# Kernel tuning notes

Hardware: AMD Instinct MI355X
Metric: run time of the kernel (lower is better)

Reference implementation:

```python
import jax, jax.numpy as jnp
import numpy as np

ROPE_BASE = 1000000.0
EPS = 1e-6
N_HEADS = 8


def apply_rope(x, base=ROPE_BASE):
    # x: [b, s, h, d]
    b, s, h, d = x.shape
    half = d // 2
    theta = 1.0 / base ** (2 * jnp.arange(half) / d)          # [half]
    angles = jnp.arange(s)[:, None] * theta[None, :]          # [s, half]
    cos = jnp.cos(angles)[None, :, None, :]                   # [1, s, 1, half]
    sin = jnp.sin(angles)[None, :, None, :]
    x1, x2 = jnp.split(x, 2, axis=-1)
    return jnp.concatenate([x1 * cos - x2 * sin, x1 * sin + x2 * cos], axis=-1)


def setup_inputs() -> dict:
    key = jax.random.key(0)
    ks = jax.random.split(key, 5)
    b, s, dim = 2, 4096, 512
    x = jax.random.normal(ks[0], (b, s, dim), dtype=jnp.float32)
    scale = jnp.ones((dim,), dtype=jnp.float32)
    init = 1.0 / np.sqrt(dim)
    Wq = jax.random.normal(ks[1], (dim, dim), dtype=jnp.float32) * init
    Wk = jax.random.normal(ks[2], (dim, dim), dtype=jnp.float32) * init
    Wv = jax.random.normal(ks[3], (dim, dim), dtype=jnp.float32) * init
    Wo = jax.random.normal(ks[4], (dim, dim), dtype=jnp.float32) * init
    return {"x": x, "scale": scale, "Wq": Wq, "Wk": Wk, "Wv": Wv, "Wo": Wo}


def reference(x, scale, Wq, Wk, Wv, Wo):
    b, s, dim = x.shape
    h = N_HEADS
    dh = dim // h
    # RMSNorm (use_fast_variance=False path)
    variance = jnp.mean(x ** 2, axis=-1, keepdims=True)
    x_norm = x / jnp.sqrt(variance + EPS) * scale
    # Projections (flax Linear: y = x @ kernel, kernel [in, out])
    q = (x_norm @ Wq).reshape(b, s, h, dh)
    k = (x_norm @ Wk).reshape(b, s, h, dh)
    v = (x_norm @ Wv).reshape(b, s, h, dh)
    q = apply_rope(q)
    k = apply_rope(k)
    scores = jnp.einsum('bthd,bshd->bhts', q, k) / jnp.sqrt(jnp.float32(dh))
    mask = jnp.triu(jnp.full((s, s), -jnp.inf, dtype=jnp.float32), k=1)
    scores = scores + mask[None, None, :, :]
    attn = jax.nn.softmax(scores, axis=-1)
    out = jnp.einsum('bhts,bshd->bthd', attn, v).reshape(b, s, dim)
    return out @ Wo
```

## Files before the change

### kernel.cpp

```cpp
#include <hip/hip_runtime.h>
#include <hip/hip_bf16.h>

typedef _Float16 f16;
typedef _Float16 f16x4 __attribute__((ext_vector_type(4)));
typedef _Float16 f16x8 __attribute__((ext_vector_type(8)));
typedef float f32x4 __attribute__((ext_vector_type(4)));

#define S_LEN 4096
#define DIM   512
#define NH    8
#define DH    64
#define BATCH 2
#define BHDIM (BATCH*NH)

#define QSCALE 0.18033688011112042f

__device__ __forceinline__ void gld16(const f16* g, f16* l) {
#if __has_builtin(__builtin_amdgcn_global_load_lds)
  __builtin_amdgcn_global_load_lds((const __attribute__((address_space(1))) void*)g,
                                   (__attribute__((address_space(3))) void*)l, 16, 0, 0);
#else
  *(f16x8*)l = *(const f16x8*)g;
#endif
}

__device__ __forceinline__ float fexp2(float x) {
#if __has_builtin(__builtin_amdgcn_exp2f)
  return __builtin_amdgcn_exp2f(x);
#else
  return exp2f(x);
#endif
}

__global__ __launch_bounds__(256) void rmsnorm_kernel(
    const float* __restrict__ x, const float* __restrict__ scale,
    f16* __restrict__ xn) {
  int row = blockIdx.x;
  int tid = threadIdx.x;
  const float* xr = x + (size_t)row * DIM;
  float2 v = *(const float2*)(xr + tid*2);
  float ss = v.x*v.x + v.y*v.y;
  #pragma unroll
  for (int off = 32; off > 0; off >>= 1) ss += __shfl_down(ss, off);
  __shared__ float red[4];
  if ((tid & 63) == 0) red[tid >> 6] = ss;
  __syncthreads();
  float tot = red[0] + red[1] + red[2] + red[3];
  float inv = rsqrtf(tot * (1.0f/DIM) + 1e-6f);
  float2 s = *(const float2*)(scale + tid*2);
  xn[(size_t)row*DIM + tid*2+0] = (f16)(v.x*inv*s.x);
  xn[(size_t)row*DIM + tid*2+1] = (f16)(v.y*inv*s.y);
}

__global__ void transpose_kernel(const float* __restrict__ Wq,
                                 const float* __restrict__ Wk,
                                 const float* __restrict__ Wv,
                                 const float* __restrict__ Wo,
                                 f16* __restrict__ wt_qkv, f16* __restrict__ wo_t) {
  __shared__ f16 tile[32][33];
  int mat = blockIdx.z;
  const float* src = (mat == 0) ? Wq : (mat == 1) ? Wk : (mat == 2) ? Wv : Wo;
  f16* dst = (mat < 3) ? (wt_qkv + (size_t)mat*DIM*DIM) : wo_t;
  int k0 = blockIdx.y * 32, n0 = blockIdx.x * 32;
  int tx = threadIdx.x, ty = threadIdx.y;
  #pragma unroll
  for (int i = 0; i < 32; i += 8)
    tile[ty+i][tx] = (f16)src[(size_t)(k0+ty+i)*DIM + n0+tx];
  __syncthreads();
  #pragma unroll
  for (int i = 0; i < 32; i += 8)
    dst[(size_t)(n0+ty+i)*DIM + k0+tx] = tile[tx][ty+i];
}

__global__ __launch_bounds__(256) void rope_table_kernel(float* __restrict__ ctab,
                                                         float* __restrict__ stab) {
  int idx = blockIdx.x*256 + threadIdx.x;
  int t = idx >> 5, d = idx & 31;
  float theta = exp2f(-(float)d * (19.931568569324174f / 32.0f));
  float sv, cv;
  sincosf((float)t * theta, &sv, &cv);
  ctab[idx] = cv; stab[idx] = sv;
}

__device__ __forceinline__ void gemm128_acc(
    const f16* __restrict__ A, const f16* __restrict__ Bt,
    int m0, int n0, f16* As, f16* Bs, f32x4 (&acc)[4][4]) {
  const int tid = threadIdx.x;
  const int wave = tid >> 6, lane = tid & 63;
  const int l16 = lane & 15, quad = lane >> 4;
  const int mrow = (wave & 1) * 64, ncol = (wave >> 1) * 64;
  const int srow = tid >> 3;
  const int gc = (tid & 7) ^ ((tid >> 3) & 7);

  for (int k0 = 0; k0 < DIM; k0 += 64) {
    if (k0) __syncthreads();
    #pragma unroll
    for (int i = 0; i < 4; i++) {
      gld16(A  + (size_t)(m0 + i*32 + srow)*DIM + k0 + gc*8, As + i*2048 + tid*8);
      gld16(Bt + (size_t)(n0 + i*32 + srow)*DIM + k0 + gc*8, Bs + i*2048 + tid*8);
    }
    __syncthreads();
    #pragma unroll
    for (int kc = 0; kc < 2; kc++) {
      f16x8 a[4], b[4];
      #pragma unroll
      for (int mt = 0; mt < 4; mt++) {
        int row = mrow + mt*16 + l16;
        a[mt] = *(const f16x8*)(As + row*64 + (((quad + 4*kc) ^ (l16 & 7)) * 8));
      }
      #pragma unroll
      for (int nt = 0; nt < 4; nt++) {
        int row = ncol + nt*16 + l16;
        b[nt] = *(const f16x8*)(Bs + row*64 + (((quad + 4*kc) ^ (l16 & 7)) * 8));
      }
      #pragma unroll
      for (int mt = 0; mt < 4; mt++)
        #pragma unroll
        for (int nt = 0; nt < 4; nt++)
          acc[mt][nt] = __builtin_amdgcn_mfma_f32_16x16x32_f16(a[mt], b[nt], acc[mt][nt], 0, 0, 0);
    }
  }
}

__global__ __launch_bounds__(256) void qkv_gemm_kernel(
    const f16* __restrict__ xn, const f16* __restrict__ wt,
    const float* __restrict__ ctab, const float* __restrict__ stab,
    f16* __restrict__ qbuf, f16* __restrict__ kbuf, f16* __restrict__ vt) {
  __shared__ __align__(16) f16 As[128*64], Bs[128*64];
  int m0 = blockIdx.x * 128, n0 = blockIdx.y * 128;
  f32x4 acc[4][4] = {};
  gemm128_acc(xn, wt, m0, n0, As, Bs, acc);

  const int tid = threadIdx.x;
  const int wave = tid >> 6, lane = tid & 63;
  const int l16 = lane & 15, quad = lane >> 4;
  int ncol = n0 + (wave >> 1) * 64;
  int which = ncol >> 9;
  int head = (ncol >> 6) & 7;
  int mbase = m0 + (wave & 1) * 64;

  if (which <= 1) {
    #pragma unroll
    for (int mt = 0; mt < 4; mt++)
      #pragma unroll
      for (int nt = 0; nt < 2; nt++) {
        int d = nt*16 + l16;
        #pragma unroll
        for (int r = 0; r < 4; r++) {
          int t = (mbase + mt*16 + quad*4 + r) & 4095;
          float cv = ctab[t*32 + d], sv = stab[t*32 + d];
          float x1 = acc[mt][nt][r], x2 = acc[mt][nt+2][r];
          acc[mt][nt][r]   = x1*cv - x2*sv;
          acc[mt][nt+2][r] = x1*sv + x2*cv;
        }
      }
  }
  if (which < 2) {
    float osc = (which == 0) ? QSCALE : 1.0f;
    f16* dst = which ? kbuf : qbuf;
    #pragma unroll
    for (int mt = 0; mt < 4; mt++)
      #pragma unroll
      for (int nt = 0; nt < 4; nt++)
        #pragma unroll
        for (int r = 0; r < 4; r++) {
          int m = mbase + mt*16 + quad*4 + r;
          int b = m >> 12, t = m & 4095;
          dst[(((size_t)(b*NH + head))*S_LEN + t)*DH + nt*16 + l16] = (f16)(acc[mt][nt][r]*osc);
        }
  } else {
    #pragma unroll
    for (int mt = 0; mt < 4; mt++)
      #pragma unroll
      for (int nt = 0; nt < 4; nt++) {
        int m = mbase + mt*16 + quad*4;
        int b = m >> 12, t = m & 4095;
        int d = nt*16 + l16;
        f16x4 v4 = {(f16)acc[mt][nt][0], (f16)acc[mt][nt][1],
                    (f16)acc[mt][nt][2], (f16)acc[mt][nt][3]};
        *(f16x4*)(vt + ((size_t)((b*NH + head)*DH + d))*S_LEN + t) = v4;
      }
  }
}

__global__ __launch_bounds__(128, 2) void attn_kernel(
    const f16* __restrict__ qbuf, const f16* __restrict__ kbuf,
    const f16* __restrict__ vtb, f16* __restrict__ ao) {
  int bid = blockIdx.x;
  int bh  = bid & 15;
  int g   = bid >> 4;
  int r4 = g >> 4, j = g & 15;
  int qhalf = (r4 == 0) ? (63 - j) : (r4 == 1) ? (32 + j)
            : (r4 == 2) ? (31 - j) : j;

  int tid = threadIdx.x;
  int wave = tid >> 6, lane = tid & 63;
  int l16 = lane & 15, quad = lane >> 4;

  const f16* Q = qbuf + (size_t)bh*S_LEN*DH;
  const f16* K = kbuf + (size_t)bh*S_LEN*DH;
  const f16* V = vtb  + (size_t)bh*DH*S_LEN;

  int rw = qhalf*64 + wave*32;
  int ntiles = qhalf + 1;
  int ntl = 2*wave + 2;
  int kcl = wave + 1;

  f16x8 qa[2][2];
  #pragma unroll
  for (int mf = 0; mf < 2; mf++) {
    const f16* qrow = Q + (size_t)(rw + mf*16 + l16)*DH + quad*8;
    qa[mf][0] = *(const f16x8*)(qrow);
    qa[mf][1] = *(const f16x8*)(qrow + 32);
  }

  f32x4 o[2][4] = {};
  float m_i[2] = {-1e30f, -1e30f};
  float l_i[2] = {0.f, 0.f};

  __shared__ __align__(16) f16 kt[2*4096];
  __shared__ __align__(16) f16 vs[2*4096];
  __shared__ __align__(16) f16 pls[2*2048];

  const int gcs = (tid & 7) ^ ((tid >> 3) & 7);
  const int srow = tid >> 3;

  #define STAGE(buf, kv)                                                        \
    do {                                                                        \
      f16* ktb = kt + (buf)*4096;                                               \
      f16* vsb = vs + (buf)*4096;                                               \
      _Pragma("unroll")                                                         \
      for (int n = 0; n < 4; n++) {                                             \
        gld16(K + (size_t)((kv) + n*16 + srow)*DH + gcs*8, ktb + n*1024 + tid*8);\
        gld16(V + (size_t)(n*16 + srow)*S_LEN + (kv) + gcs*8, vsb + n*1024 + tid*8);\
      }                                                                         \
    } while (0)

  STAGE(0, 0);
  __syncthreads();

  for (int it = 0; it < ntiles; ++it) {
    int kv0 = it * 64;
    int cur = it & 1;
    bool last = (it == ntiles - 1);
    if (!last) STAGE(cur ^ 1, kv0 + 64);

    const f16* ktc = kt + cur*4096;
    const f16* vsc = vs + cur*4096;

    f32x4 st[2][4];
    #pragma unroll
    for (int nt = 0; nt < 4; nt++) {
      if (!(last && nt >= ntl)) {
        int row = nt*16 + l16;
        f16x8 kf0 = *(const f16x8*)(ktc + row*64 + (((quad)     ^ (row & 7))*8));
        f16x8 kf1 = *(const f16x8*)(ktc + row*64 + (((quad + 4) ^ (row & 7))*8));
        f32x4 z0 = {}, z1 = {};
        z0 = __builtin_amdgcn_mfma_f32_16x16x32_f16(kf0, qa[0][0], z0, 0, 0, 0);
        z1 = __builtin_amdgcn_mfma_f32_16x16x32_f16(kf0, qa[1][0], z1, 0, 0, 0);
        st[0][nt] = __builtin_amdgcn_mfma_f32_16x16x32_f16(kf1, qa[0][1], z0, 0, 0, 0);
        st[1][nt] = __builtin_amdgcn_mfma_f32_16x16x32_f16(kf1, qa[1][1], z1, 0, 0, 0);
      }
    }

    #pragma unroll
    for (int mf = 0; mf < 2; mf++) {
      int qrow = rw + mf*16 + l16;
      float rmx = -1e30f;
      if (last) {
        #pragma unroll
        for (int nt = 0; nt < 4; nt++) {
          if (nt >= ntl) continue;
          int kbase = kv0 + nt*16 + quad*4;
          #pragma unroll
          for (int r = 0; r < 4; r++) {
            float v = st[mf][nt][r];
            if (kbase + r > qrow) v = -1e30f;
            st[mf][nt][r] = v;
            rmx = fmaxf(rmx, v);
          }
        }
      } else {
        #pragma unroll
        for (int nt = 0; nt < 4; nt++)
          #pragma unroll
          for (int r = 0; r < 4; r++) rmx = fmaxf(rmx, st[mf][nt][r]);
      }
      rmx = fmaxf(rmx, __shfl_xor(rmx, 16));
      rmx = fmaxf(rmx, __shfl_xor(rmx, 32));
      if (!__all(rmx <= m_i[mf] + 8.0f)) {
        float mnew = fmaxf(m_i[mf], rmx);
        float alpha = fexp2(m_i[mf] - mnew);
        m_i[mf] = mnew;
        float al[4];
        #pragma unroll
        for (int r = 0; r < 4; r++) al[r] = __shfl(alpha, quad*4 + r);
        #pragma unroll
        for (int dnt = 0; dnt < 4; dnt++)
          #pragma unroll
          for (int r = 0; r < 4; r++) o[mf][dnt][r] *= al[r];
        l_i[mf] *= alpha;
      }
      float mref = m_i[mf];
      float rs = 0.f;
      f16* plw = pls + wave*2048 + mf*1024 + l16*64;
      #pragma unroll
      for (int nt = 0; nt < 4; nt++) {
        if (last && nt >= ntl) continue;
        f16x4 p4;
        #pragma unroll
        for (int r = 0; r < 4; r++) {
          float p = fexp2(st[mf][nt][r] - mref);
          rs += p;
          p4[r] = (f16)p;
        }
        int cw = nt*2 + (quad >> 1);
        *(f16x4*)(plw + ((cw ^ (l16 & 7))*8) + (quad & 1)*4) = p4;
      }
      rs += __shfl_xor(rs, 16);
      rs += __shfl_xor(rs, 32);
      l_i[mf] += rs;
    }

    #pragma unroll
    for (int kc = 0; kc < 2; kc++) {
      if (last && kc >= kcl) continue;
      int cp = ((kc*4 + quad) ^ (l16 & 7))*8;
      f16x8 pa0 = *(const f16x8*)(pls + wave*2048 +        l16*64 + cp);
      f16x8 pa1 = *(const f16x8*)(pls + wave*2048 + 1024 + l16*64 + cp);
      #pragma unroll
      for (int dnt = 0; dnt < 4; dnt++) {
        int vrow2 = dnt*16 + l16;
        f16x8 vf = *(const f16x8*)(vsc + vrow2*64 + (((kc*4 + quad) ^ (vrow2 & 7))*8));
        o[0][dnt] = __builtin_amdgcn_mfma_f32_16x16x32_f16(pa0, vf, o[0][dnt], 0, 0, 0);
        o[1][dnt] = __builtin_amdgcn_mfma_f32_16x16x32_f16(pa1, vf, o[1][dnt], 0, 0, 0);
      }
    }

    __syncthreads();
  }
  #undef STAGE

  int b = bh >> 3, h = bh & 7;
  #pragma unroll
  for (int mf = 0; mf < 2; mf++) {
    float lr[4];
    #pragma unroll
    for (int r = 0; r < 4; r++) lr[r] = __shfl(l_i[mf], quad*4 + r);
    #pragma unroll
    for (int r = 0; r < 4; r++) {
      float invl = 1.0f / lr[r];
      int t = rw + mf*16 + quad*4 + r;
      size_t rowoff = ((size_t)(b*S_LEN + t))*DIM + h*DH;
      #pragma unroll
      for (int dnt = 0; dnt < 4; dnt++)
        ao[rowoff + dnt*16 + l16] = (f16)(o[mf][dnt][r]*invl);
    }
  }
}

__global__ __launch_bounds__(256) void out_gemm_kernel(
    const f16* __restrict__ ao, const f16* __restrict__ wot,
    float* __restrict__ out) {
  __shared__ __align__(16) f16 As[128*64], Bs[128*64];
  int m0 = blockIdx.x * 128, n0 = blockIdx.y * 128;
  f32x4 acc[4][4] = {};
  gemm128_acc(ao, wot, m0, n0, As, Bs, acc);

  const int tid = threadIdx.x;
  const int wave = tid >> 6, lane = tid & 63;
  const int l16 = lane & 15, quad = lane >> 4;
  int ncol = n0 + (wave >> 1) * 64;
  int mbase = m0 + (wave & 1) * 64;
  #pragma unroll
  for (int mt = 0; mt < 4; mt++)
    #pragma unroll
    for (int nt = 0; nt < 4; nt++)
      #pragma unroll
      for (int r = 0; r < 4; r++)
        out[(size_t)(mbase + mt*16 + quad*4 + r)*DIM + ncol + nt*16 + l16] = acc[mt][nt][r];
}

extern "C" void kernel_launch(void* const* d_in, const int* in_sizes, int n_in,
                              void* d_out, int out_size, void* d_ws, size_t ws_size,
                              hipStream_t stream) {
  const float* x     = (const float*)d_in[0];
  const float* scale = (const float*)d_in[1];
  const float* Wq    = (const float*)d_in[2];
  const float* Wk    = (const float*)d_in[3];
  const float* Wv    = (const float*)d_in[4];
  const float* Wo    = (const float*)d_in[5];
  float* out = (float*)d_out;

  const size_t ROWS = (size_t)BATCH * S_LEN;
  char* ws = (char*)d_ws;
  f16* xn     = (f16*)ws;  ws += ROWS * DIM * sizeof(f16);
  f16* wt_qkv = (f16*)ws;  ws += (size_t)3 * DIM * DIM * sizeof(f16);
  f16* wo_t   = (f16*)ws;  ws += (size_t)DIM * DIM * sizeof(f16);
  f16* qb     = (f16*)ws;  ws += (size_t)BHDIM * S_LEN * DH * sizeof(f16);
  f16* kb     = (f16*)ws;  ws += (size_t)BHDIM * S_LEN * DH * sizeof(f16);
  f16* vt     = (f16*)ws;  ws += (size_t)BHDIM * S_LEN * DH * sizeof(f16);
  float* ctab = (float*)ws; ws += (size_t)S_LEN * 32 * sizeof(float);
  float* stab = (float*)ws; ws += (size_t)S_LEN * 32 * sizeof(float);
  f16* ao     = xn;

  size_t need = (size_t)(ws - (char*)d_ws);
  if (ws_size < need) return;

  rmsnorm_kernel   <<<ROWS, 256, 0, stream>>>(x, scale, xn);
  transpose_kernel <<<dim3(16,16,4), dim3(32,8), 0, stream>>>(Wq, Wk, Wv, Wo, wt_qkv, wo_t);
  rope_table_kernel<<<512, 256, 0, stream>>>(ctab, stab);
  qkv_gemm_kernel  <<<dim3(64,12), 256, 0, stream>>>(xn, wt_qkv, ctab, stab, qb, kb, vt);
  attn_kernel      <<<1024, 128, 0, stream>>>(qb, kb, vt, ao);
  out_gemm_kernel  <<<dim3(64,4), 256, 0, stream>>>(ao, wo_t, out);
}
```

Before: 214.7 us.

## Pair mirrored 32-row query bands per block to balance causal attention work

```diff
diff --git a/kernel.cpp b/kernel.cpp
--- a/kernel.cpp
+++ b/kernel.cpp
@@ -188,10 +188,7 @@
     const f16* __restrict__ vtb, f16* __restrict__ ao) {
   int bid = blockIdx.x;
   int bh  = bid & 15;
-  int g   = bid >> 4;
-  int r4 = g >> 4, j = g & 15;
-  int qhalf = (r4 == 0) ? (63 - j) : (r4 == 1) ? (32 + j)
-            : (r4 == 2) ? (31 - j) : j;
+  int p   = bid >> 4;
 
   int tid = threadIdx.x;
   int wave = tid >> 6, lane = tid & 63;
@@ -201,17 +198,16 @@
   const f16* K = kbuf + (size_t)bh*S_LEN*DH;
   const f16* V = vtb  + (size_t)bh*DH*S_LEN;
 
-  int rw = qhalf*64 + wave*32;
-  int ntiles = qhalf + 1;
-  int ntl = 2*wave + 2;
-  int kcl = wave + 1;
+  int bandv[2] = {127 - p, p};
+  int tcnt[2]  = {((127 - p) >> 1) + 1, (p >> 1) + 1};
+  int rbase[2] = {bandv[0]*32 + wave*16, bandv[1]*32 + wave*16};
 
   f16x8 qa[2][2];
   #pragma unroll
-  for (int mf = 0; mf < 2; mf++) {
-    const f16* qrow = Q + (size_t)(rw + mf*16 + l16)*DH + quad*8;
-    qa[mf][0] = *(const f16x8*)(qrow);
-    qa[mf][1] = *(const f16x8*)(qrow + 32);
+  for (int bi = 0; bi < 2; bi++) {
+    const f16* qrow = Q + (size_t)(rbase[bi] + l16)*DH + quad*8;
+    qa[bi][0] = *(const f16x8*)(qrow);
+    qa[bi][1] = *(const f16x8*)(qrow + 32);
   }
 
   f32x4 o[2][4] = {};
@@ -220,7 +216,7 @@
 
   __shared__ __align__(16) f16 kt[2*4096];
   __shared__ __align__(16) f16 vs[2*4096];
-  __shared__ __align__(16) f16 pls[2*2048];
+  __shared__ __align__(16) f16 pls[4096];
 
   const int gcs = (tid & 7) ^ ((tid >> 3) & 7);
   const int srow = tid >> 3;
@@ -239,101 +235,107 @@
   STAGE(0, 0);
   __syncthreads();
 
-  for (int it = 0; it < ntiles; ++it) {
+  int nth = tcnt[0];
+  for (int it = 0; it < nth; ++it) {
     int kv0 = it * 64;
     int cur = it & 1;
-    bool last = (it == ntiles - 1);
-    if (!last) STAGE(cur ^ 1, kv0 + 64);
+    if (it + 1 < nth) STAGE(cur ^ 1, kv0 + 64);
 
     const f16* ktc = kt + cur*4096;
     const f16* vsc = vs + cur*4096;
 
-    f32x4 st[2][4];
-    #pragma unroll
-    for (int nt = 0; nt < 4; nt++) {
-      if (!(last && nt >= ntl)) {
+    bool act1 = (it < tcnt[1]);
+    bool dia[2] = {it == tcnt[0] - 1, it == tcnt[1] - 1};
+
+    #pragma unroll
+    for (int bi = 0; bi < 2; bi++) {
+      if (bi == 1 && !act1) continue;
+      bool diag = dia[bi];
+      int ntl = diag ? ((bandv[bi] & 1) ? 4 : 2) : 4;
+
+      f32x4 st[4];
+      #pragma unroll
+      for (int nt = 0; nt < 4; nt++) {
+        if (nt >= ntl) continue;
         int row = nt*16 + l16;
         f16x8 kf0 = *(const f16x8*)(ktc + row*64 + (((quad)     ^ (row & 7))*8));
         f16x8 kf1 = *(const f16x8*)(ktc + row*64 + (((quad + 4) ^ (row & 7))*8));
-        f32x4 z0 = {}, z1 = {};
-        z0 = __builtin_amdgcn_mfma_f32_16x16x32_f16(kf0, qa[0][0], z0, 0, 0, 0);
-        z1 = __builtin_amdgcn_mfma_f32_16x16x32_f16(kf0, qa[1][0], z1, 0, 0, 0);
-        st[0][nt] = __builtin_amdgcn_mfma_f32_16x16x32_f16(kf1, qa[0][1], z0, 0, 0, 0);
-        st[1][nt] = __builtin_amdgcn_mfma_f32_16x16x32_f16(kf1, qa[1][1], z1, 0, 0, 0);
-      }
-    }
-
-    #pragma unroll
-    for (int mf = 0; mf < 2; mf++) {
-      int qrow = rw + mf*16 + l16;
+        f32x4 z = {};
+        z = __builtin_amdgcn_mfma_f32_16x16x32_f16(kf0, qa[bi][0], z, 0, 0, 0);
+        st[nt] = __builtin_amdgcn_mfma_f32_16x16x32_f16(kf1, qa[bi][1], z, 0, 0, 0);
+      }
+
+      int qglob = rbase[bi] + l16;
       float rmx = -1e30f;
-      if (last) {
-        #pragma unroll
-        for (int nt = 0; nt < 4; nt++) {
-          if (nt >= ntl) continue;
-          int kbase = kv0 + nt*16 + quad*4;
+      #pragma unroll
+      for (int nt = 0; nt < 4; nt++) {
+        if (nt >= ntl) continue;
+        if (diag) {
+          int kb = kv0 + nt*16 + quad*4;
           #pragma unroll
           for (int r = 0; r < 4; r++) {
-            float v = st[mf][nt][r];
-            if (kbase + r > qrow) v = -1e30f;
-            st[mf][nt][r] = v;
+            float v = st[nt][r];
+            if (kb + r > qglob) v = -1e30f;
+            st[nt][r] = v;
             rmx = fmaxf(rmx, v);
           }
+        } else {
+          #pragma unroll
+          for (int r = 0; r < 4; r++) rmx = fmaxf(rmx, st[nt][r]);
         }
-      } else {
-        #pragma unroll
-        for (int nt = 0; nt < 4; nt++)
-          #pragma unroll
-          for (int r = 0; r < 4; r++) rmx = fmaxf(rmx, st[mf][nt][r]);
       }
       rmx = fmaxf(rmx, __shfl_xor(rmx, 16));
       rmx = fmaxf(rmx, __shfl_xor(rmx, 32));
-      if (!__all(rmx <= m_i[mf] + 8.0f)) {
-        float mnew = fmaxf(m_i[mf], rmx);
-        float alpha = fexp2(m_i[mf] - mnew);
-        m_i[mf] = mnew;
+      if (!__all(rmx <= m_i[bi] + 8.0f)) {
+        float mnew = fmaxf(m_i[bi], rmx);
+        float alpha = fexp2(m_i[bi] - mnew);
+        m_i[bi] = mnew;
         float al[4];
         #pragma unroll
         for (int r = 0; r < 4; r++) al[r] = __shfl(alpha, quad*4 + r);
         #pragma unroll
         for (int dnt = 0; dnt < 4; dnt++)
           #pragma unroll
-          for (int r = 0; r < 4; r++) o[mf][dnt][r] *= al[r];
-        l_i[mf] *= alpha;
-      }
-      float mref = m_i[mf];
+          for (int r = 0; r < 4; r++) o[bi][dnt][r] *= al[r];
+        l_i[bi] *= alpha;
+      }
+      float mref = m_i[bi];
       float rs = 0.f;
-      f16* plw = pls + wave*2048 + mf*1024 + l16*64;
+      f16* plw = pls + wave*2048 + bi*1024 + l16*64;
       #pragma unroll
       for (int nt = 0; nt < 4; nt++) {
-        if (last && nt >= ntl) continue;
+        if (nt >= ntl) continue;
         f16x4 p4;
         #pragma unroll
         for (int r = 0; r < 4; r++) {
-          float p = fexp2(st[mf][nt][r] - mref);
-          rs += p;
-          p4[r] = (f16)p;
+          float pv = fexp2(st[nt][r] - mref);
+          rs += pv;
+          p4[r] = (f16)pv;
         }
         int cw = nt*2 + (quad >> 1);
         *(f16x4*)(plw + ((cw ^ (l16 & 7))*8) + (quad & 1)*4) = p4;
       }
       rs += __shfl_xor(rs, 16);
       rs += __shfl_xor(rs, 32);
-      l_i[mf] += rs;
+      l_i[bi] += rs;
     }
 
+    int kcl0 = dia[0] ? ((bandv[0] & 1) ? 2 : 1) : 2;
+    int kcl1 = act1 ? (dia[1] ? ((bandv[1] & 1) ? 2 : 1) : 2) : 0;
     #pragma unroll
     for (int kc = 0; kc < 2; kc++) {
-      if (last && kc >= kcl) continue;
+      bool lv0 = (kc < kcl0), lv1 = (kc < kcl1);
+      if (!lv0 && !lv1) continue;
       int cp = ((kc*4 + quad) ^ (l16 & 7))*8;
-      f16x8 pa0 = *(const f16x8*)(pls + wave*2048 +        l16*64 + cp);
-      f16x8 pa1 = *(const f16x8*)(pls + wave*2048 + 1024 + l16*64 + cp);
+      f16x8 pa0, pa1;
+      if (lv0) pa0 = *(const f16x8*)(pls + wave*2048 +        l16*64 + cp);
+      if (lv1) pa1 = *(const f16x8*)(pls + wave*2048 + 1024 + l16*64 + cp);
       #pragma unroll
       for (int dnt = 0; dnt < 4; dnt++) {
-        int vrow2 = dnt*16 + l16;
-        f16x8 vf = *(const f16x8*)(vsc + vrow2*64 + (((kc*4 + quad) ^ (vrow2 & 7))*8));
-        o[0][dnt] = __builtin_amdgcn_mfma_f32_16x16x32_f16(pa0, vf, o[0][dnt], 0, 0, 0);
-        o[1][dnt] = __builtin_amdgcn_mfma_f32_16x16x32_f16(pa1, vf, o[1][dnt], 0, 0, 0);
+        int vr = dnt*16 + l16;
+        f16x8 vf = *(const f16x8*)(vsc + vr*64 + (((kc*4 + quad) ^ (vr & 7))*8));
+        if (lv0) o[0][dnt] = __builtin_amdgcn_mfma_f32_16x16x32_f16(pa0, vf, o[0][dnt], 0, 0, 0);
+        if (lv1) o[1][dnt] = __builtin_amdgcn_mfma_f32_16x16x32_f16(pa1, vf, o[1][dnt], 0, 0, 0);
       }
     }
 
@@ -343,18 +345,18 @@
 
   int b = bh >> 3, h = bh & 7;
   #pragma unroll
-  for (int mf = 0; mf < 2; mf++) {
+  for (int bi = 0; bi < 2; bi++) {
     float lr[4];
     #pragma unroll
-    for (int r = 0; r < 4; r++) lr[r] = __shfl(l_i[mf], quad*4 + r);
+    for (int r = 0; r < 4; r++) lr[r] = __shfl(l_i[bi], quad*4 + r);
     #pragma unroll
     for (int r = 0; r < 4; r++) {
       float invl = 1.0f / lr[r];
-      int t = rw + mf*16 + quad*4 + r;
+      int t = rbase[bi] + quad*4 + r;
       size_t rowoff = ((size_t)(b*S_LEN + t))*DIM + h*DH;
       #pragma unroll
       for (int dnt = 0; dnt < 4; dnt++)
-        ao[rowoff + dnt*16 + l16] = (f16)(o[mf][dnt][r]*invl);
+        ao[rowoff + dnt*16 + l16] = (f16)(o[bi][dnt][r]*invl);
     }
   }
 }
```

Result: no change. 211.0 us (-1.7%).
